# Kernel optimization log

Measured on AMD Instinct MI355X. Metric: run time of the kernel, lower is better.

Reference implementation:

```python
import jax, jax.numpy as jnp
import numpy as np

B, T, I, H, O = 8192, 180, 7, 64, 16

def setup_inputs() -> dict:
    key = jax.random.key(0)
    ks = jax.random.split(key, 8)
    s_ih = 1.0 / np.sqrt(H)
    x = jax.random.normal(ks[0], (B, T, I), dtype=jnp.float32)
    # PyTorch nn.LSTM param layout: [4H, in] with gate order i, f, g, o
    W_ih = jax.random.uniform(ks[1], (4 * H, I), jnp.float32, -s_ih, s_ih)
    W_hh = jax.random.uniform(ks[2], (4 * H, H), jnp.float32, -s_ih, s_ih)
    b_ih = jax.random.uniform(ks[3], (4 * H,), jnp.float32, -s_ih, s_ih)
    b_hh = jax.random.uniform(ks[4], (4 * H,), jnp.float32, -s_ih, s_ih)
    W_fc = jax.random.uniform(ks[5], (O, H), jnp.float32, -s_ih, s_ih)
    b_fc = jax.random.uniform(ks[6], (O,), jnp.float32, -s_ih, s_ih)
    return {"x": x, "W_ih": W_ih, "W_hh": W_hh, "b_ih": b_ih,
            "b_hh": b_hh, "W_fc": W_fc, "b_fc": b_fc}

def reference(x, W_ih, W_hh, b_ih, b_hh, W_fc, b_fc):
    x = x.reshape(-1, T, I)
    b = b_ih + b_hh
    # precompute input projections for all timesteps: [T, B, 4H]
    xg = jnp.einsum('bti,gi->tbg', x, W_ih) + b

    def step(carry, xg_t):
        h, c = carry
        gates = xg_t + h @ W_hh.T  # [B, 4H]
        i_g, f_g, g_g, o_g = jnp.split(gates, 4, axis=-1)
        i_g = jax.nn.sigmoid(i_g)
        f_g = jax.nn.sigmoid(f_g)
        g_g = jnp.tanh(g_g)
        o_g = jax.nn.sigmoid(o_g)
        c = f_g * c + i_g * g_g
        h = o_g * jnp.tanh(c)
        return (h, c), None

    h0 = jnp.zeros((x.shape[0], H), dtype=x.dtype)
    c0 = jnp.zeros((x.shape[0], H), dtype=x.dtype)
    (h_last, _), _ = jax.lax.scan(step, (h0, c0), xg)
    return h_last @ W_fc.T + b_fc  # [B, O]
```

## Files before the change

kernel.cpp:

```cpp
#include <hip/hip_runtime.h>
#include <math.h>

#ifndef __has_builtin
#define __has_builtin(x) 0
#endif

#if __has_builtin(__builtin_amdgcn_rcpf)
#define FAST_RCP(x) __builtin_amdgcn_rcpf(x)
#else
#define FAST_RCP(x) (1.0f / (x))
#endif

#if __has_builtin(__builtin_amdgcn_exp2f)
#define FAST_EXP2(x) __builtin_amdgcn_exp2f(x)
#else
#define FAST_EXP2(x) exp2f(x)
#endif

typedef _Float16 half8 __attribute__((ext_vector_type(8)));
typedef _Float16 half2v __attribute__((ext_vector_type(2)));
typedef float f32x4 __attribute__((ext_vector_type(4)));
typedef float f32x2 __attribute__((ext_vector_type(2)));

constexpr int T_STEPS = 180;
constexpr int I_DIM   = 7;
constexpr int HDIM    = 64;
constexpr int BT      = 16;
constexpr int NCH     = 12;
constexpr int CH_HALF = BT * 8;
constexpr int XSTR    = 136;

__global__ __launch_bounds__(512, 4) void lstm_mfma_kernel(
    const float* __restrict__ x,
    const float* __restrict__ W_ih,
    const float* __restrict__ W_hh,
    const float* __restrict__ b_ih,
    const float* __restrict__ b_hh,
    const float* __restrict__ W_fc,
    const float* __restrict__ b_fc,
    float* __restrict__ out) {
    __shared__ alignas(16) _Float16 Bbuf[2][NCH][BT][8];
    __shared__ alignas(16) _Float16 xstage[T_STEPS * XSTR];
    __shared__ alignas(16) float hlds[BT][HDIM + 4];

    const int tid  = (int)threadIdx.x;
    const int w    = tid >> 6;
    const int lane = tid & 63;
    const int q    = lane >> 4;
    const int n15  = lane & 15;
    const long bbase = (long)blockIdx.x * BT;

    half8 afrag[2][3];
#pragma unroll
    for (int pt = 0; pt < 2; ++pt) {
        const int rq   = n15 >> 2;
        const int gate = n15 & 3;
        const int unit = 8 * w + 2 * rq + pt;
        const int grow = gate * HDIM + unit;
        const float scl = (gate == 2) ? 2.88539008177792681472f
                                      : -1.44269504088896340736f;
#pragma unroll
        for (int kc = 0; kc < 3; ++kc) {
#pragma unroll
            for (int j = 0; j < 8; ++j) {
                const int k = kc * 32 + q * 8 + j;
                float v;
                if (k < I_DIM)            v = W_ih[grow * I_DIM + k];
                else if (k == I_DIM)      v = b_ih[grow] + b_hh[grow];
                else if (k < 8 + HDIM)    v = W_hh[grow * HDIM + (k - 8)];
                else                      v = 0.0f;
                afrag[pt][kc][j] = (_Float16)(scl * v);
            }
        }
    }

    for (int idx = tid; idx < BT * T_STEPS * I_DIM; idx += 512) {
        const int n = idx / (T_STEPS * I_DIM);
        const int r = idx - n * (T_STEPS * I_DIM);
        const int t = r / I_DIM, i = r - t * I_DIM;
        xstage[t * XSTR + n * 8 + i] =
            (_Float16)x[(bbase + n) * (T_STEPS * I_DIM) + r];
    }
    for (int idx = tid; idx < T_STEPS * BT; idx += 512)
        xstage[(idx >> 4) * XSTR + (idx & 15) * 8 + 7] = (_Float16)1.0f;
    for (int idx = tid; idx < 2 * NCH * CH_HALF; idx += 512)
        ((_Float16*)Bbuf)[idx] = (_Float16)0.0f;
    __syncthreads();

    const int u0 = 8 * w + 2 * q;

    const _Float16* const rb0 = &Bbuf[0][q][n15][0];
    const _Float16* const rb1 = &Bbuf[1][q][n15][0];
    const _Float16* xb0 = (q == 0) ? &xstage[0 * XSTR + n15 * 8] : rb0;
    const _Float16* xb1 = (q == 0) ? &xstage[1 * XSTR + n15 * 8] : rb1;
    const int xadv = (q == 0) ? 2 * XSTR : 0;
    half2v* const hw0 = (half2v*)&Bbuf[0][1 + w][n15][2 * q];
    half2v* const hw1 = (half2v*)&Bbuf[1][1 + w][n15][2 * q];

    float c0 = 0.0f, c1 = 0.0f, h0 = 0.0f, h1 = 0.0f;

#define LSTM_CELL(ACC, CREG, HREG)                                             \
    {                                                                          \
        const float A = FAST_EXP2(ACC[0]);                                     \
        const float F = FAST_EXP2(ACC[1]);                                     \
        const float E = FAST_EXP2(ACC[2]);                                     \
        const float P = (1.0f + A) * (E + 1.0f);                               \
        const float Q = 1.0f + F;                                              \
        const float R = FAST_RCP(P * Q);                                       \
        CREG = (CREG * P + (E - 1.0f) * Q) * R;                                \
        const float O = FAST_EXP2(ACC[3]);                                     \
        float cs = 2.88539008177792681472f * CREG;                             \
        cs = fminf(fmaxf(cs, -80.0f), 80.0f);                                  \
        const float C = FAST_EXP2(cs);                                         \
        HREG = (C - 1.0f) * FAST_RCP((1.0f + O) * (C + 1.0f));                 \
    }

#define LSTM_STEP(RB, XB, HW)                                                  \
    {                                                                          \
        const half8 bf0 = *(const half8*)(XB);                                 \
        const half8 bf1 = *(const half8*)((RB) + 4 * CH_HALF);                 \
        const half8 bf2 = *(const half8*)((RB) + 8 * CH_HALF);                 \
        f32x4 acc0 = {0.f, 0.f, 0.f, 0.f};                                     \
        f32x4 acc1 = {0.f, 0.f, 0.f, 0.f};                                     \
        acc0 = __builtin_amdgcn_mfma_f32_16x16x32_f16(afrag[0][0], bf0, acc0, 0, 0, 0); \
        acc1 = __builtin_amdgcn_mfma_f32_16x16x32_f16(afrag[1][0], bf0, acc1, 0, 0, 0); \
        acc0 = __builtin_amdgcn_mfma_f32_16x16x32_f16(afrag[0][1], bf1, acc0, 0, 0, 0); \
        acc1 = __builtin_amdgcn_mfma_f32_16x16x32_f16(afrag[1][1], bf1, acc1, 0, 0, 0); \
        acc0 = __builtin_amdgcn_mfma_f32_16x16x32_f16(afrag[0][2], bf2, acc0, 0, 0, 0); \
        acc1 = __builtin_amdgcn_mfma_f32_16x16x32_f16(afrag[1][2], bf2, acc1, 0, 0, 0); \
        LSTM_CELL(acc0, c0, h0)                                                \
        LSTM_CELL(acc1, c1, h1)                                                \
        *(HW) = (half2v){(_Float16)h0, (_Float16)h1};                          \
        __syncthreads();                                                       \
    }

    for (int t = 0; t < T_STEPS; t += 2) {
        LSTM_STEP(rb0, xb0, hw1)
        LSTM_STEP(rb1, xb1, hw0)
        xb0 += xadv;
        xb1 += xadv;
    }
#undef LSTM_STEP
#undef LSTM_CELL

    *(f32x2*)&hlds[n15][u0] = (f32x2){h0, h1};
    __syncthreads();
    if (tid < 256) {
        const int b = tid >> 4, j = tid & 15;
        float s = b_fc[j];
#pragma unroll 8
        for (int u = 0; u < HDIM; ++u)
            s += hlds[b][u] * W_fc[j * HDIM + u];
        out[(bbase + b) * 16 + j] = s;
    }
}

extern "C" void kernel_launch(void* const* d_in, const int* in_sizes, int n_in,
                              void* d_out, int out_size, void* d_ws, size_t ws_size,
                              hipStream_t stream) {
    const float* x    = (const float*)d_in[0];
    const float* W_ih = (const float*)d_in[1];
    const float* W_hh = (const float*)d_in[2];
    const float* b_ih = (const float*)d_in[3];
    const float* b_hh = (const float*)d_in[4];
    const float* W_fc = (const float*)d_in[5];
    const float* b_fc = (const float*)d_in[6];
    float* out = (float*)d_out;

    const int B = in_sizes[0] / (T_STEPS * I_DIM);
    const int grid = B / BT;

    lstm_mfma_kernel<<<grid, 512, 0, stream>>>(x, W_ih, W_hh, b_ih, b_hh,
                                               W_fc, b_fc, out);
}
```

Measured before the change: 196.8 us.

## Split LSTM hidden units across 16 waves with one unit per lane

Each block now runs 1024 threads (16 waves) instead of 512, so every lane handles one hidden unit rather than two. This halves the serial MFMA chain and gate math per wave on each timestep. The K-chain is also split into two independent accumulators that are summed, to shorten MFMA dependency latency. The x staging loop is merged so the bias-ones column is written in the same pass. The cost is more waves taking part in every per-step __syncthreads barrier, and possibly fewer resident blocks per CU.

```diff
diff --git a/kernel.cpp b/kernel.cpp
--- a/kernel.cpp
+++ b/kernel.cpp
@@ -18,7 +18,6 @@
 #endif
 
 typedef _Float16 half8 __attribute__((ext_vector_type(8)));
-typedef _Float16 half2v __attribute__((ext_vector_type(2)));
 typedef float f32x4 __attribute__((ext_vector_type(4)));
 typedef float f32x2 __attribute__((ext_vector_type(2)));
 
@@ -30,7 +29,7 @@
 constexpr int CH_HALF = BT * 8;
 constexpr int XSTR    = 136;
 
-__global__ __launch_bounds__(512, 4) void lstm_mfma_kernel(
+__global__ __launch_bounds__(1024, 8) void lstm_mfma_kernel(
     const float* __restrict__ x,
     const float* __restrict__ W_ih,
     const float* __restrict__ W_hh,
@@ -50,12 +49,10 @@
     const int n15  = lane & 15;
     const long bbase = (long)blockIdx.x * BT;
 
-    half8 afrag[2][3];
-#pragma unroll
-    for (int pt = 0; pt < 2; ++pt) {
-        const int rq   = n15 >> 2;
+    half8 afrag[3];
+    {
         const int gate = n15 & 3;
-        const int unit = 8 * w + 2 * rq + pt;
+        const int unit = 4 * w + (n15 >> 2);
         const int grow = gate * HDIM + unit;
         const float scl = (gate == 2) ? 2.88539008177792681472f
                                       : -1.44269504088896340736f;
@@ -69,37 +66,38 @@
                 else if (k == I_DIM)      v = b_ih[grow] + b_hh[grow];
                 else if (k < 8 + HDIM)    v = W_hh[grow * HDIM + (k - 8)];
                 else                      v = 0.0f;
-                afrag[pt][kc][j] = (_Float16)(scl * v);
+                afrag[kc][j] = (_Float16)(scl * v);
             }
         }
     }
 
-    for (int idx = tid; idx < BT * T_STEPS * I_DIM; idx += 512) {
-        const int n = idx / (T_STEPS * I_DIM);
-        const int r = idx - n * (T_STEPS * I_DIM);
-        const int t = r / I_DIM, i = r - t * I_DIM;
-        xstage[t * XSTR + n * 8 + i] =
-            (_Float16)x[(bbase + n) * (T_STEPS * I_DIM) + r];
+    for (int idx = tid; idx < BT * T_STEPS * 8; idx += 1024) {
+        const int i = idx & 7;
+        const int n = (idx >> 3) & 15;
+        const int t = idx >> 7;
+        float v = 1.0f;
+        if (i < I_DIM)
+            v = x[(bbase + n) * (T_STEPS * I_DIM) + t * I_DIM + i];
+        xstage[t * XSTR + n * 8 + i] = (_Float16)v;
     }
-    for (int idx = tid; idx < T_STEPS * BT; idx += 512)
-        xstage[(idx >> 4) * XSTR + (idx & 15) * 8 + 7] = (_Float16)1.0f;
-    for (int idx = tid; idx < 2 * NCH * CH_HALF; idx += 512)
+    for (int idx = tid; idx < 2 * NCH * CH_HALF; idx += 1024)
         ((_Float16*)Bbuf)[idx] = (_Float16)0.0f;
     __syncthreads();
 
-    const int u0 = 8 * w + 2 * q;
+    const int u = 4 * w + q;
 
     const _Float16* const rb0 = &Bbuf[0][q][n15][0];
     const _Float16* const rb1 = &Bbuf[1][q][n15][0];
     const _Float16* xb0 = (q == 0) ? &xstage[0 * XSTR + n15 * 8] : rb0;
     const _Float16* xb1 = (q == 0) ? &xstage[1 * XSTR + n15 * 8] : rb1;
     const int xadv = (q == 0) ? 2 * XSTR : 0;
-    half2v* const hw0 = (half2v*)&Bbuf[0][1 + w][n15][2 * q];
-    half2v* const hw1 = (half2v*)&Bbuf[1][1 + w][n15][2 * q];
+    _Float16* const hw0 = &Bbuf[0][1 + (u >> 3)][n15][u & 7];
+    _Float16* const hw1 = &Bbuf[1][1 + (u >> 3)][n15][u & 7];
 
-    float c0 = 0.0f, c1 = 0.0f, h0 = 0.0f, h1 = 0.0f;
+    float c = 0.0f, h = 0.0f;
+    const f32x4 zq = {0.0f, 0.0f, 0.0f, 0.0f};
 
-#define LSTM_CELL(ACC, CREG, HREG)                                             \
+#define LSTM_CELL(ACC)                                                         \
     {                                                                          \
         const float A = FAST_EXP2(ACC[0]);                                     \
         const float F = FAST_EXP2(ACC[1]);                                     \
@@ -107,12 +105,12 @@
         const float P = (1.0f + A) * (E + 1.0f);                               \
         const float Q = 1.0f + F;                                              \
         const float R = FAST_RCP(P * Q);                                       \
-        CREG = (CREG * P + (E - 1.0f) * Q) * R;                                \
+        c = (c * P + (E - 1.0f) * Q) * R;                                      \
         const float O = FAST_EXP2(ACC[3]);                                     \
-        float cs = 2.88539008177792681472f * CREG;                             \
+        float cs = 2.88539008177792681472f * c;                                \
         cs = fminf(fmaxf(cs, -80.0f), 80.0f);                                  \
         const float C = FAST_EXP2(cs);                                         \
-        HREG = (C - 1.0f) * FAST_RCP((1.0f + O) * (C + 1.0f));                 \
+        h = (C - 1.0f) * FAST_RCP((1.0f + O) * (C + 1.0f));                    \
     }
 
 #define LSTM_STEP(RB, XB, HW)                                                  \
@@ -120,17 +118,12 @@
         const half8 bf0 = *(const half8*)(XB);                                 \
         const half8 bf1 = *(const half8*)((RB) + 4 * CH_HALF);                 \
         const half8 bf2 = *(const half8*)((RB) + 8 * CH_HALF);                 \
-        f32x4 acc0 = {0.f, 0.f, 0.f, 0.f};                                     \
-        f32x4 acc1 = {0.f, 0.f, 0.f, 0.f};                                     \
-        acc0 = __builtin_amdgcn_mfma_f32_16x16x32_f16(afrag[0][0], bf0, acc0, 0, 0, 0); \
-        acc1 = __builtin_amdgcn_mfma_f32_16x16x32_f16(afrag[1][0], bf0, acc1, 0, 0, 0); \
-        acc0 = __builtin_amdgcn_mfma_f32_16x16x32_f16(afrag[0][1], bf1, acc0, 0, 0, 0); \
-        acc1 = __builtin_amdgcn_mfma_f32_16x16x32_f16(afrag[1][1], bf1, acc1, 0, 0, 0); \
-        acc0 = __builtin_amdgcn_mfma_f32_16x16x32_f16(afrag[0][2], bf2, acc0, 0, 0, 0); \
-        acc1 = __builtin_amdgcn_mfma_f32_16x16x32_f16(afrag[1][2], bf2, acc1, 0, 0, 0); \
-        LSTM_CELL(acc0, c0, h0)                                                \
-        LSTM_CELL(acc1, c1, h1)                                                \
-        *(HW) = (half2v){(_Float16)h0, (_Float16)h1};                          \
+        f32x4 accA = __builtin_amdgcn_mfma_f32_16x16x32_f16(afrag[0], bf0, zq, 0, 0, 0); \
+        f32x4 accB = __builtin_amdgcn_mfma_f32_16x16x32_f16(afrag[2], bf2, zq, 0, 0, 0); \
+        accA = __builtin_amdgcn_mfma_f32_16x16x32_f16(afrag[1], bf1, accA, 0, 0, 0); \
+        const f32x4 acc = accA + accB;                                         \
+        LSTM_CELL(acc)                                                         \
+        *(HW) = (_Float16)h;                                                   \
         __syncthreads();                                                       \
     }
 
@@ -143,14 +136,14 @@
 #undef LSTM_STEP
 #undef LSTM_CELL
 
-    *(f32x2*)&hlds[n15][u0] = (f32x2){h0, h1};
+    hlds[n15][u] = h;
     __syncthreads();
     if (tid < 256) {
         const int b = tid >> 4, j = tid & 15;
         float s = b_fc[j];
 #pragma unroll 8
-        for (int u = 0; u < HDIM; ++u)
-            s += hlds[b][u] * W_fc[j * HDIM + u];
+        for (int uu = 0; uu < HDIM; ++uu)
+            s += hlds[b][uu] * W_fc[j * HDIM + uu];
         out[(bbase + b) * 16 + j] = s;
     }
 }
@@ -170,6 +163,6 @@
     const int B = in_sizes[0] / (T_STEPS * I_DIM);
     const int grid = B / BT;
 
-    lstm_mfma_kernel<<<grid, 512, 0, stream>>>(x, W_ih, W_hh, b_ih, b_hh,
-                                               W_fc, b_fc, out);
+    lstm_mfma_kernel<<<grid, 1024, 0, stream>>>(x, W_ih, W_hh, b_ih, b_hh,
+                                                W_fc, b_fc, out);
 }
```

Result: slower. 226.5 us (+15.1%).
